# Optimization experiments

Hardware: AMD Instinct MI355X
Metric: run time of the kernel (lower is better)

The kernel has to match this reference:

```python
import jax, jax.numpy as jnp
import numpy as np

S, G, NMUL, LENF = 730, 4000, 2, 15
NEARZERO = 1e-5

# param bounds (change_param_range: lb + raw*(ub-lb)), raw in [0,1]
HBV_LB = np.array([1., 50., .05, .01, .001, .2, 0., 0., -2.5, .5, 0., 0.], np.float32)
HBV_UB = np.array([6., 1000., .9, .5, .2, 1., 10., 100., 2.5, 10., .1, .2], np.float32)
EXP_LB = np.array([0., 100., 10., 0., 0., -3.], np.float32)
EXP_UB = np.array([.1, 1500., 50., 5., 3., 0.], np.float32)


def _descale(raw, lb, ub):
    # raw: [G, n_par, NMUL]
    return lb[None, :, None] + raw * (ub - lb)[None, :, None]


def _hbv(P, T, PET, ph):
    # ph: [G,12,NMUL]; order: beta fc k0 k1 k2 lp perc uzl tt cfmax cfr cwh
    beta, fc, k0, k1, k2, lp, perc, uzl, tt, cfmax, cfr, cwh = [ph[:, i, :] for i in range(12)]

    def step(carry, inp):
        sp, mw, sm, suz, slz = carry
        p, t, pet = inp
        rain = jnp.where(t >= tt, p, 0.)
        sp = sp + jnp.where(t < tt, p, 0.)
        melt = jnp.minimum(jnp.maximum(cfmax * (t - tt), 0.), sp)
        mw = mw + melt; sp = sp - melt
        refr = jnp.minimum(jnp.maximum(cfr * cfmax * (tt - t), 0.), mw)
        sp = sp + refr; mw = mw - refr
        tosoil = jnp.maximum(mw - cwh * sp, 0.)
        mw = mw - tosoil
        sw = jnp.clip((sm / fc) ** beta, 0., 1.)
        rech = (rain + tosoil) * sw
        sm = sm + rain + tosoil - rech
        excess = jnp.maximum(sm - fc, 0.); sm = sm - excess
        et = jnp.minimum(pet * jnp.clip(sm / (lp * fc), 0., 1.), sm)
        sm = jnp.maximum(sm - et, NEARZERO)
        suz = suz + rech + excess
        pa = jnp.minimum(perc, suz); suz = suz - pa
        q0 = k0 * jnp.maximum(suz - uzl, 0.); suz = suz - q0
        q1 = k1 * suz; suz = suz - q1
        slz = slz + pa
        q2 = k2 * slz; slz = slz - q2
        return (sp, mw, sm, suz, slz), q0 + q1 + q2

    z = jnp.full_like(fc, NEARZERO)
    init = (z, z, 0.5 * fc, z, z)
    _, q = jax.lax.scan(step, init, (P, T, PET))
    return q  # [S,G,NMUL]


def _exphydro(P, T, PET, pe):
    # pe: [G,6,NMUL]; order: f smax qmax df tmax tmin
    f, smax, qmax, df, tmax, tmin = [pe[:, i, :] for i in range(6)]

    def step(carry, inp):
        s0, s1 = carry
        p, t, pet = inp
        ps = jnp.where(t <= tmin, p, 0.)
        pr = p - ps
        melt = jnp.where(t > tmax, jnp.minimum(s0, df * (t - tmax)), 0.)
        s0 = s0 + ps - melt
        s1 = s1 + pr + melt
        qspill = jnp.maximum(s1 - smax, 0.); s1 = s1 - qspill
        et = jnp.minimum(pet * jnp.clip(s1 / smax, 0., 1.), s1); s1 = s1 - et
        qb = jnp.minimum(qmax * jnp.exp(-f * jnp.maximum(smax - s1, 0.)), s1)
        s1 = s1 - qb
        return (s0, s1), qspill + qb

    z = jnp.full_like(smax, NEARZERO)
    init = (z, 0.5 * smax)
    _, q = jax.lax.scan(step, init, (P, T, PET))
    return q  # [S,G,NMUL]


def _uh_gamma(a, b):
    # a,b: [G]; gamma-pdf unit hydrograph, lenF=LENF
    aa = jax.nn.relu(a) + 0.1
    th = jax.nn.relu(b) + 0.5
    t = jnp.arange(LENF, dtype=jnp.float32) + 0.5  # [LENF]
    logw = (-jax.scipy.special.gammaln(aa)[None, :] - aa[None, :] * jnp.log(th)[None, :]
            + (aa - 1.)[None, :] * jnp.log(t)[:, None] - t[:, None] / th[None, :])
    w = jnp.exp(logw)
    return w / w.sum(0, keepdims=True)  # [LENF,G]


def _route(q, w):
    # causal depthwise conv: out[t,g] = sum_k w[k,g] * q[t-k,g]
    qp = jnp.pad(q, ((LENF - 1, 0), (0, 0)))
    out = jnp.zeros_like(q)
    for k in range(LENF):
        out = out + w[k][None, :] * qp[LENF - 1 - k: LENF - 1 - k + q.shape[0]]
    return out


def setup_inputs() -> dict:
    key = jax.random.key(0)
    k1, k2 = jax.random.split(key)
    u = jax.random.uniform(k1, (S, G, 3), dtype=jnp.float32)
    # physical forcing ranges: prcp [0,10] mm/d, tmean [-10,20] C, pet [0,5] mm/d
    x = jnp.stack([u[..., 0] * 10., u[..., 1] * 30. - 10., u[..., 2] * 5.], axis=-1)
    raw_phy_static = jax.random.uniform(k2, (G, 18 * NMUL + 2), dtype=jnp.float32)
    return {"x": x, "raw_phy_static": raw_phy_static}


def reference(x, raw_phy_static):
    # unpack: [G, 18*NMUL] static block + 2 routing params
    static = raw_phy_static[:, :18 * NMUL].reshape(G, 18, NMUL)
    ph = _descale(static[:, :12, :], jnp.asarray(HBV_LB), jnp.asarray(HBV_UB))
    pe = _descale(static[:, 12:, :], jnp.asarray(EXP_LB), jnp.asarray(EXP_UB))
    route = raw_phy_static[:, 18 * NMUL:]
    rout_a = route[:, 0] * 2.9   # bounds [0, 2.9]
    rout_b = route[:, 1] * 6.5   # bounds [0, 6.5]

    P = jnp.broadcast_to(x[:, :, 0, None], (S, G, NMUL))
    T = jnp.broadcast_to(x[:, :, 1, None], (S, G, NMUL))
    PET = jnp.broadcast_to(x[:, :, 2, None], (S, G, NMUL))

    q_hbv = _hbv(P, T, PET, ph)
    q_exp = _exphydro(P, T, PET, pe)
    qsim = 0.5 * (q_hbv.mean(-1) + q_exp.mean(-1))  # blend over models, mean over nmul -> [S,G]

    w = _uh_gamma(rout_a, rout_b)
    return _route(qsim, w)  # [S,G] routed streamflow
```

## Files before the change

kernel.cpp:

```cpp
#include <hip/hip_runtime.h>

#define SS 730
#define GG 4000
#define LENF 15
#define PD 10
#define GPAD 4032
#define TT 10
#define QN ((size_t)SS * GG)

template<bool STORE4>
__global__ __launch_bounds__(64) void hydro_scan(const float* __restrict__ x,
                                                 const float* __restrict__ raw,
                                                 float* __restrict__ qsim) {
    int tid = blockIdx.x * 64 + threadIdx.x;
    int g = tid % GPAD;
    int inst = tid / GPAD;
    if (g >= GG) return;
    int m = inst & 1;
    const float* xg = x + (size_t)g * 3;
    const float* pr = raw + (size_t)g * 38 + m;

    float* qp = qsim + (STORE4 ? (size_t)inst * QN : 0) + g;

    float pb[PD], tb[PD], eb[PD];
#pragma unroll
    for (int j = 0; j < PD; ++j) {
        const float* xn = xg + (size_t)j * (3 * GG);
        pb[j] = xn[0]; tb[j] = xn[1]; eb[j] = xn[2];
    }

    if (inst < 2) {
        float beta  = 1.0f   + pr[0]  * 5.0f;
        float fc    = 50.0f  + pr[2]  * 950.0f;
        float k0    = 0.05f  + pr[4]  * 0.85f;
        float k1    = 0.01f  + pr[6]  * 0.49f;
        float k2    = 0.001f + pr[8]  * 0.199f;
        float lp    = 0.2f   + pr[10] * 0.8f;
        float perc  =          pr[12] * 10.0f;
        float uzl   =          pr[14] * 100.0f;
        float tt    = -2.5f  + pr[16] * 5.0f;
        float cfmax = 0.5f   + pr[18] * 9.5f;
        float cfr   =          pr[20] * 0.1f;
        float cwh   =          pr[22] * 0.2f;
        float invfc   = 1.0f / fc;
        float invlpfc = 1.0f / (lp * fc);
        float cfrcf   = cfr * cfmax;

        float sp = 1e-5f, mw = 1e-5f, sm = 0.5f * fc, suz = 1e-5f, slz = 1e-5f;

        auto body = [&](float p, float tc, float pet) -> float {
            float rain = (tc >= tt) ? p : 0.0f;
            float snow = (tc <  tt) ? p : 0.0f;
            sp += snow;
            float melt = fminf(fmaxf(cfmax * (tc - tt), 0.0f), sp);
            mw += melt; sp -= melt;
            float refr = fminf(fmaxf(cfrcf * (tt - tc), 0.0f), mw);
            sp += refr; mw -= refr;
            float tosoil = fmaxf(mw - cwh * sp, 0.0f);
            mw -= tosoil;
            float sw = fminf(exp2f(beta * __log2f(sm * invfc)), 1.0f);
            float rt = rain + tosoil;
            float rech = rt * sw;
            sm += rt - rech;
            float excess = fmaxf(sm - fc, 0.0f);
            sm -= excess;
            float et = fminf(pet * fminf(fmaxf(sm * invlpfc, 0.0f), 1.0f), sm);
            sm = fmaxf(sm - et, 1e-5f);
            suz += rech + excess;
            float pa = fminf(perc, suz);
            suz -= pa;
            float q0 = k0 * fmaxf(suz - uzl, 0.0f);
            suz -= q0;
            float q1 = k1 * suz;
            suz -= q1;
            slz += pa;
            float q2 = k2 * slz;
            slz -= q2;
            return q0 + q1 + q2;
        };

        const float* xpre = xg + (size_t)PD * (3 * GG);
        for (int c = 0; c < SS / PD - 1; ++c) {
#pragma unroll
            for (int j = 0; j < PD; ++j) {
                float p = pb[j], tc = tb[j], pet = eb[j];
                pb[j] = xpre[0]; tb[j] = xpre[1]; eb[j] = xpre[2];
                xpre += 3 * GG;
                float q = body(p, tc, pet);
                if (STORE4) *qp = q; else atomicAdd(qp, 0.25f * q);
                qp += GG;
            }
        }
#pragma unroll
        for (int j = 0; j < PD; ++j) {
            float q = body(pb[j], tb[j], eb[j]);
            if (STORE4) *qp = q; else atomicAdd(qp, 0.25f * q);
            qp += GG;
        }
    } else {
        const float* pe = pr + 24;
        float f    =           pe[0]  * 0.1f;
        float smax = 100.0f  + pe[2]  * 1400.0f;
        float qmax = 10.0f   + pe[4]  * 40.0f;
        float df   =           pe[6]  * 5.0f;
        float tmax =           pe[8]  * 3.0f;
        float tmin = -3.0f   + pe[10] * 3.0f;
        float invsmax = 1.0f / smax;

        float s0 = 1e-5f, s1 = 0.5f * smax;

        auto body = [&](float p, float tc, float pet) -> float {
            float ps  = (tc <= tmin) ? p : 0.0f;
            float prr = p - ps;
            float melt = (tc > tmax) ? fminf(s0, df * (tc - tmax)) : 0.0f;
            s0 += ps - melt;
            s1 += prr + melt;
            float qspill = fmaxf(s1 - smax, 0.0f);
            s1 -= qspill;
            float et = fminf(pet * fminf(fmaxf(s1 * invsmax, 0.0f), 1.0f), s1);
            s1 -= et;
            float qb = fminf(qmax * expf(-f * fmaxf(smax - s1, 0.0f)), s1);
            s1 -= qb;
            return qspill + qb;
        };

        const float* xpre = xg + (size_t)PD * (3 * GG);
        for (int c = 0; c < SS / PD - 1; ++c) {
#pragma unroll
            for (int j = 0; j < PD; ++j) {
                float p = pb[j], tc = tb[j], pet = eb[j];
                pb[j] = xpre[0]; tb[j] = xpre[1]; eb[j] = xpre[2];
                xpre += 3 * GG;
                float q = body(p, tc, pet);
                if (STORE4) *qp = q; else atomicAdd(qp, 0.25f * q);
                qp += GG;
            }
        }
#pragma unroll
        for (int j = 0; j < PD; ++j) {
            float q = body(pb[j], tb[j], eb[j]);
            if (STORE4) *qp = q; else atomicAdd(qp, 0.25f * q);
            qp += GG;
        }
    }
}

template<int NB>
__global__ __launch_bounds__(256) void hydro_route(const float* __restrict__ qsim,
                                                   const float* __restrict__ raw,
                                                   float* __restrict__ out) {
    int idx = blockIdx.x * 256 + threadIdx.x;
    if (idx >= GG * (SS / TT)) return;
    int g = idx % GG;
    int c = idx / GG;
    int t0 = c * TT;

    float a = raw[(size_t)g * 38 + 36] * 2.9f;
    float b = raw[(size_t)g * 38 + 37] * 6.5f;
    float aa = fmaxf(a, 0.0f) + 0.1f;
    float th = fmaxf(b, 0.0f) + 0.5f;
    float am1 = aa - 1.0f;
    float invth = 1.0f / th;

    const float logt[LENF] = {
        -0.69314718f, 0.40546511f, 0.91629073f, 1.25276297f, 1.50407740f,
         1.70474809f, 1.87180218f, 2.01490302f, 2.14006616f, 2.25129180f,
         2.35137526f, 2.44234704f, 2.52572864f, 2.60268969f, 2.67414865f };

    float w[LENF];
    float s = 0.0f;
#pragma unroll
    for (int k = 0; k < LENF; ++k) {
        float tk = (float)k + 0.5f;
        w[k] = expf(am1 * logt[k] - tk * invth);
        s += w[k];
    }
    float scale = (NB == 4 ? 0.25f : 1.0f) / s;

    float v[TT + LENF - 1];
#pragma unroll
    for (int i = 0; i < TT + LENF - 1; ++i) {
        int tp = t0 - (LENF - 1) + i;
        float sv = 0.0f;
        if (tp >= 0) {
            const float* qb = qsim + (size_t)tp * GG + g;
            sv = qb[0];
            if (NB == 4) sv += qb[QN] + qb[2 * QN] + qb[3 * QN];
        }
        v[i] = sv;
    }
#pragma unroll
    for (int j = 0; j < TT; ++j) {
        float acc = 0.0f;
#pragma unroll
        for (int k = 0; k < LENF; ++k)
            acc += w[k] * v[j + (LENF - 1) - k];
        out[(size_t)(t0 + j) * GG + g] = acc * scale;
    }
}

extern "C" void kernel_launch(void* const* d_in, const int* in_sizes, int n_in,
                              void* d_out, int out_size, void* d_ws, size_t ws_size,
                              hipStream_t stream) {
    const float* x   = (const float*)d_in[0];
    const float* raw = (const float*)d_in[1];
    float* out  = (float*)d_out;
    float* qsim = (float*)d_ws;

    if (ws_size >= 4 * QN * sizeof(float)) {
        hydro_scan<true><<<(4 * GPAD) / 64, 64, 0, stream>>>(x, raw, qsim);
        hydro_route<4><<<(GG * (SS / TT) + 255) / 256, 256, 0, stream>>>(qsim, raw, out);
    } else {
        hipMemsetAsync(qsim, 0, QN * sizeof(float), stream);
        hydro_scan<false><<<(4 * GPAD) / 64, 64, 0, stream>>>(x, raw, qsim);
        hydro_route<1><<<(GG * (SS / TT) + 255) / 256, 256, 0, stream>>>(qsim, raw, out);
    }
}
```

Baseline: 125.9 us.

## Fuse HBV and EXP-Hydro scans into one thread per basin-member

Each thread now runs both the HBV and EXP-Hydro recurrences for one (basin, nmul) pair and writes their summed output. This halves the scan threads and the intermediate qsim traffic, from four planes to two, and the routing kernel reads two planes instead of four. The input forcing loads are shared by both models. The cost is a longer serial dependency chain per thread and fewer total threads (about 8000) to hide latency. The EXP-Hydro exp is also rewritten as exp2 with a prescaled constant.

```diff
diff --git a/kernel.cpp b/kernel.cpp
--- a/kernel.cpp
+++ b/kernel.cpp
@@ -4,23 +4,50 @@
 #define GG 4000
 #define LENF 15
 #define PD 10
-#define GPAD 4032
 #define TT 10
 #define QN ((size_t)SS * GG)
 
-template<bool STORE4>
+template<bool STORE2>
 __global__ __launch_bounds__(64) void hydro_scan(const float* __restrict__ x,
                                                  const float* __restrict__ raw,
                                                  float* __restrict__ qsim) {
     int tid = blockIdx.x * 64 + threadIdx.x;
-    int g = tid % GPAD;
-    int inst = tid / GPAD;
-    if (g >= GG) return;
-    int m = inst & 1;
+    if (tid >= 2 * GG) return;
+    int g = tid % GG;
+    int m = tid / GG;
     const float* xg = x + (size_t)g * 3;
     const float* pr = raw + (size_t)g * 38 + m;
 
-    float* qp = qsim + (STORE4 ? (size_t)inst * QN : 0) + g;
+    float* qp = qsim + (STORE2 ? (size_t)m * QN : 0) + g;
+
+    float beta  = 1.0f   + pr[0]  * 5.0f;
+    float fc    = 50.0f  + pr[2]  * 950.0f;
+    float k0    = 0.05f  + pr[4]  * 0.85f;
+    float k1    = 0.01f  + pr[6]  * 0.49f;
+    float k2    = 0.001f + pr[8]  * 0.199f;
+    float lp    = 0.2f   + pr[10] * 0.8f;
+    float perc  =          pr[12] * 10.0f;
+    float uzl   =          pr[14] * 100.0f;
+    float tt    = -2.5f  + pr[16] * 5.0f;
+    float cfmax = 0.5f   + pr[18] * 9.5f;
+    float cfr   =          pr[20] * 0.1f;
+    float cwh   =          pr[22] * 0.2f;
+    float invfc   = 1.0f / fc;
+    float invlpfc = 1.0f / (lp * fc);
+    float cfrcf   = cfr * cfmax;
+
+    const float* pe = pr + 24;
+    float f    =           pe[0]  * 0.1f;
+    float smax = 100.0f  + pe[2]  * 1400.0f;
+    float qmax = 10.0f   + pe[4]  * 40.0f;
+    float df   =           pe[6]  * 5.0f;
+    float tmax =           pe[8]  * 3.0f;
+    float tmin = -3.0f   + pe[10] * 3.0f;
+    float invsmax = 1.0f / smax;
+    float fl = f * 1.44269504f;
+
+    float sp = 1e-5f, mw = 1e-5f, sm = 0.5f * fc, suz = 1e-5f, slz = 1e-5f;
+    float s0 = 1e-5f, s1 = 0.5f * smax;
 
     float pb[PD], tb[PD], eb[PD];
 #pragma unroll
@@ -29,119 +56,67 @@
         pb[j] = xn[0]; tb[j] = xn[1]; eb[j] = xn[2];
     }
 
-    if (inst < 2) {
-        float beta  = 1.0f   + pr[0]  * 5.0f;
-        float fc    = 50.0f  + pr[2]  * 950.0f;
-        float k0    = 0.05f  + pr[4]  * 0.85f;
-        float k1    = 0.01f  + pr[6]  * 0.49f;
-        float k2    = 0.001f + pr[8]  * 0.199f;
-        float lp    = 0.2f   + pr[10] * 0.8f;
-        float perc  =          pr[12] * 10.0f;
-        float uzl   =          pr[14] * 100.0f;
-        float tt    = -2.5f  + pr[16] * 5.0f;
-        float cfmax = 0.5f   + pr[18] * 9.5f;
-        float cfr   =          pr[20] * 0.1f;
-        float cwh   =          pr[22] * 0.2f;
-        float invfc   = 1.0f / fc;
-        float invlpfc = 1.0f / (lp * fc);
-        float cfrcf   = cfr * cfmax;
+    auto body = [&](float p, float tc, float pet) -> float {
+        float rain = (tc >= tt) ? p : 0.0f;
+        float snow = p - rain;
+        sp += snow;
+        float melt = fminf(fmaxf(cfmax * (tc - tt), 0.0f), sp);
+        mw += melt; sp -= melt;
+        float refr = fminf(fmaxf(cfrcf * (tt - tc), 0.0f), mw);
+        sp += refr; mw -= refr;
+        float tosoil = fmaxf(mw - cwh * sp, 0.0f);
+        mw -= tosoil;
+        float sw = fminf(exp2f(beta * __log2f(sm * invfc)), 1.0f);
+        float rt = rain + tosoil;
+        float rech = rt * sw;
+        sm += rt - rech;
+        float excess = fmaxf(sm - fc, 0.0f);
+        sm -= excess;
+        float et = fminf(pet * fminf(fmaxf(sm * invlpfc, 0.0f), 1.0f), sm);
+        sm = fmaxf(sm - et, 1e-5f);
+        suz += rech + excess;
+        float pa = fminf(perc, suz);
+        suz -= pa;
+        float q0 = k0 * fmaxf(suz - uzl, 0.0f);
+        suz -= q0;
+        float q1 = k1 * suz;
+        suz -= q1;
+        slz += pa;
+        float q2 = k2 * slz;
+        slz -= q2;
 
-        float sp = 1e-5f, mw = 1e-5f, sm = 0.5f * fc, suz = 1e-5f, slz = 1e-5f;
+        float ps  = (tc <= tmin) ? p : 0.0f;
+        float prr = p - ps;
+        float mlt = (tc > tmax) ? fminf(s0, df * (tc - tmax)) : 0.0f;
+        s0 += ps - mlt;
+        s1 += prr + mlt;
+        float qspill = fmaxf(s1 - smax, 0.0f);
+        s1 -= qspill;
+        float ete = fminf(pet * fminf(fmaxf(s1 * invsmax, 0.0f), 1.0f), s1);
+        s1 -= ete;
+        float qb = fminf(qmax * exp2f(-fl * fmaxf(smax - s1, 0.0f)), s1);
+        s1 -= qb;
 
-        auto body = [&](float p, float tc, float pet) -> float {
-            float rain = (tc >= tt) ? p : 0.0f;
-            float snow = (tc <  tt) ? p : 0.0f;
-            sp += snow;
-            float melt = fminf(fmaxf(cfmax * (tc - tt), 0.0f), sp);
-            mw += melt; sp -= melt;
-            float refr = fminf(fmaxf(cfrcf * (tt - tc), 0.0f), mw);
-            sp += refr; mw -= refr;
-            float tosoil = fmaxf(mw - cwh * sp, 0.0f);
-            mw -= tosoil;
-            float sw = fminf(exp2f(beta * __log2f(sm * invfc)), 1.0f);
-            float rt = rain + tosoil;
-            float rech = rt * sw;
-            sm += rt - rech;
-            float excess = fmaxf(sm - fc, 0.0f);
-            sm -= excess;
-            float et = fminf(pet * fminf(fmaxf(sm * invlpfc, 0.0f), 1.0f), sm);
-            sm = fmaxf(sm - et, 1e-5f);
-            suz += rech + excess;
-            float pa = fminf(perc, suz);
-            suz -= pa;
-            float q0 = k0 * fmaxf(suz - uzl, 0.0f);
-            suz -= q0;
-            float q1 = k1 * suz;
-            suz -= q1;
-            slz += pa;
-            float q2 = k2 * slz;
-            slz -= q2;
-            return q0 + q1 + q2;
-        };
+        return (q0 + q1 + q2) + (qspill + qb);
+    };
 
-        const float* xpre = xg + (size_t)PD * (3 * GG);
-        for (int c = 0; c < SS / PD - 1; ++c) {
-#pragma unroll
-            for (int j = 0; j < PD; ++j) {
-                float p = pb[j], tc = tb[j], pet = eb[j];
-                pb[j] = xpre[0]; tb[j] = xpre[1]; eb[j] = xpre[2];
-                xpre += 3 * GG;
-                float q = body(p, tc, pet);
-                if (STORE4) *qp = q; else atomicAdd(qp, 0.25f * q);
-                qp += GG;
-            }
-        }
+    const float* xpre = xg + (size_t)PD * (3 * GG);
+    for (int c = 0; c < SS / PD - 1; ++c) {
 #pragma unroll
         for (int j = 0; j < PD; ++j) {
-            float q = body(pb[j], tb[j], eb[j]);
-            if (STORE4) *qp = q; else atomicAdd(qp, 0.25f * q);
+            float p = pb[j], tc = tb[j], pet = eb[j];
+            pb[j] = xpre[0]; tb[j] = xpre[1]; eb[j] = xpre[2];
+            xpre += 3 * GG;
+            float q = body(p, tc, pet);
+            if (STORE2) *qp = q; else atomicAdd(qp, 0.25f * q);
             qp += GG;
         }
-    } else {
-        const float* pe = pr + 24;
-        float f    =           pe[0]  * 0.1f;
-        float smax = 100.0f  + pe[2]  * 1400.0f;
-        float qmax = 10.0f   + pe[4]  * 40.0f;
-        float df   =           pe[6]  * 5.0f;
-        float tmax =           pe[8]  * 3.0f;
-        float tmin = -3.0f   + pe[10] * 3.0f;
-        float invsmax = 1.0f / smax;
-
-        float s0 = 1e-5f, s1 = 0.5f * smax;
-
-        auto body = [&](float p, float tc, float pet) -> float {
-            float ps  = (tc <= tmin) ? p : 0.0f;
-            float prr = p - ps;
-            float melt = (tc > tmax) ? fminf(s0, df * (tc - tmax)) : 0.0f;
-            s0 += ps - melt;
-            s1 += prr + melt;
-            float qspill = fmaxf(s1 - smax, 0.0f);
-            s1 -= qspill;
-            float et = fminf(pet * fminf(fmaxf(s1 * invsmax, 0.0f), 1.0f), s1);
-            s1 -= et;
-            float qb = fminf(qmax * expf(-f * fmaxf(smax - s1, 0.0f)), s1);
-            s1 -= qb;
-            return qspill + qb;
-        };
-
-        const float* xpre = xg + (size_t)PD * (3 * GG);
-        for (int c = 0; c < SS / PD - 1; ++c) {
+    }
 #pragma unroll
-            for (int j = 0; j < PD; ++j) {
-                float p = pb[j], tc = tb[j], pet = eb[j];
-                pb[j] = xpre[0]; tb[j] = xpre[1]; eb[j] = xpre[2];
-                xpre += 3 * GG;
-                float q = body(p, tc, pet);
-                if (STORE4) *qp = q; else atomicAdd(qp, 0.25f * q);
-                qp += GG;
-            }
-        }
-#pragma unroll
-        for (int j = 0; j < PD; ++j) {
-            float q = body(pb[j], tb[j], eb[j]);
-            if (STORE4) *qp = q; else atomicAdd(qp, 0.25f * q);
-            qp += GG;
-        }
+    for (int j = 0; j < PD; ++j) {
+        float q = body(pb[j], tb[j], eb[j]);
+        if (STORE2) *qp = q; else atomicAdd(qp, 0.25f * q);
+        qp += GG;
     }
 }
 
@@ -175,7 +150,7 @@
         w[k] = expf(am1 * logt[k] - tk * invth);
         s += w[k];
     }
-    float scale = (NB == 4 ? 0.25f : 1.0f) / s;
+    float scale = 0.25f / s;
 
     float v[TT + LENF - 1];
 #pragma unroll
@@ -185,7 +160,7 @@
         if (tp >= 0) {
             const float* qb = qsim + (size_t)tp * GG + g;
             sv = qb[0];
-            if (NB == 4) sv += qb[QN] + qb[2 * QN] + qb[3 * QN];
+            if (NB == 2) sv += qb[QN];
         }
         v[i] = sv;
     }
@@ -207,12 +182,12 @@
     float* out  = (float*)d_out;
     float* qsim = (float*)d_ws;
 
-    if (ws_size >= 4 * QN * sizeof(float)) {
-        hydro_scan<true><<<(4 * GPAD) / 64, 64, 0, stream>>>(x, raw, qsim);
-        hydro_route<4><<<(GG * (SS / TT) + 255) / 256, 256, 0, stream>>>(qsim, raw, out);
+    if (ws_size >= 2 * QN * sizeof(float)) {
+        hydro_scan<true><<<(2 * GG + 63) / 64, 64, 0, stream>>>(x, raw, qsim);
+        hydro_route<2><<<(GG * (SS / TT) + 255) / 256, 256, 0, stream>>>(qsim, raw, out);
     } else {
         hipMemsetAsync(qsim, 0, QN * sizeof(float), stream);
-        hydro_scan<false><<<(4 * GPAD) / 64, 64, 0, stream>>>(x, raw, qsim);
+        hydro_scan<false><<<(2 * GG + 63) / 64, 64, 0, stream>>>(x, raw, qsim);
         hydro_route<1><<<(GG * (SS / TT) + 255) / 256, 256, 0, stream>>>(qsim, raw, out);
     }
 }
```

New measurement: 154.7 us. 1.23x slower.
